# Kernel optimization log

Measured on AMD Instinct MI355X. Metric: run time of the kernel, lower is better.

## Reference

```python
import jax, jax.numpy as jnp
import numpy as np

LAM = 0.5


def _conv3x3(z, W):
    # z: [n, 2, h, w], W: [1, 2, 3, 3] (OIHW), padding=1, no bias
    return jax.lax.conv_general_dilated(
        z, W, window_strides=(1, 1), padding='SAME',
        dimension_numbers=('NCHW', 'OIHW', 'NCHW'))


def setup_inputs() -> dict:
    key = jax.random.key(0)
    k0, k1, k2, k3 = jax.random.split(key, 4)
    n, t, c, h, w = 32, 8, 128, 32, 32
    x = jax.random.normal(k0, (n, t, c, h, w), dtype=jnp.float32)
    alpha = jnp.full((1,), 0.5, dtype=jnp.float32)
    beta = jnp.full((1,), 0.5, dtype=jnp.float32)
    W_fc = jax.random.normal(k1, (t, t), dtype=jnp.float32) * (1.0 / np.sqrt(t))
    W_conv1 = jax.random.normal(k2, (1, 2, 3, 3), dtype=jnp.float32) * 0.2
    W_conv2 = jax.random.normal(k3, (1, 2, 3, 3), dtype=jnp.float32) * 0.2
    return {"x": x, "alpha": alpha, "beta": beta, "W_fc": W_fc,
            "W_conv1": W_conv1, "W_conv2": W_conv2}


def reference(x, alpha, beta, W_fc, W_conv1, W_conv2):
    n, t, c, h, w = x.shape
    # --- pooled time-channel map ---
    avg = jnp.mean(x, axis=(3, 4))            # [n,t,c]
    mx = jnp.max(x, axis=(3, 4))              # [n,t,c]
    map_add = 0.5 * (avg + mx) + alpha[0] * avg + beta[0] * mx
    # fc along time axis (Linear(t,t,bias=False) applied to [n,c,t]):
    # y[n,s,c] = sum_t map_add[n,t,c] * W_fc[s,t]
    map_add = jnp.einsum('ntc,st->nsc', map_add, W_fc)  # [n,t,c]

    kc = int(c * LAM)
    kt = int(t * LAM)
    # important channels: topk over channel axis, per timestep.
    # Faithful to the original: the fancy-index assignment unions the topk
    # selections over the batch, so the mask is batch-independent.
    _, idx_c = jax.lax.top_k(map_add, kc)                     # [n,t,kc]
    mask_c = jax.nn.one_hot(idx_c, c, dtype=x.dtype).max(axis=2).max(axis=0)  # [t,c]
    # important times: topk over time axis, per channel.
    _, idx_t = jax.lax.top_k(jnp.swapaxes(map_add, 1, 2), kt)  # [n,c,kt]
    mask_t = jax.nn.one_hot(idx_t, t, dtype=x.dtype).max(axis=2).max(axis=0).T  # [t,c]

    # torch.where((mask_c+mask_t)/2 == 0.5, 1, 0)  ==  XOR of the two masks
    im_tc = ((mask_c + mask_t) == 1.0).astype(x.dtype)  # [t,c]
    sub_tc = 1.0 - im_tc

    imf = x * im_tc[None, :, :, None, None]
    subf = x * sub_tc[None, :, :, None, None]
    imf = imf.reshape(n, t * c, h, w)
    subf = subf.reshape(n, t * c, h, w)

    im_avg = jnp.mean(imf, axis=1, keepdims=True) / LAM
    im_max = jnp.max(imf, axis=1, keepdims=True)
    sub_avg = jnp.mean(subf, axis=1, keepdims=True) / (1.0 - LAM)
    sub_max = jnp.max(subf, axis=1, keepdims=True)

    im_map = jax.nn.sigmoid(_conv3x3(jnp.concatenate([im_avg, im_max], axis=1), W_conv1))
    sub_map = jax.nn.sigmoid(_conv3x3(jnp.concatenate([sub_avg, sub_max], axis=1), W_conv2))

    out = im_map * imf + sub_map * subf                 # [n, t*c, h, w]
    return out.reshape(n, t, c, h, w)
```

## Files before the change

### kernel.cpp

```cpp
#include <hip/hip_runtime.h>
#include <math.h>

#define TC  1024
#define P_  1024
#define KC  64
#define KT  4

typedef float vfloat4 __attribute__((ext_vector_type(4)));


__global__ __launch_bounds__(256) void k1_reduce(const float* __restrict__ x,
                                                 float* __restrict__ avg,
                                                 float* __restrict__ mx,
                                                 int* __restrict__ masks) {
    int r = blockIdx.x;
    if (r == 0) {
        #pragma unroll
        for (int j = 0; j < 8; ++j) masks[j * 256 + threadIdx.x] = 0;
    }
    const float4* xp = (const float4*)(x + (size_t)r * P_);
    float4 v = xp[threadIdx.x];
    float s = (v.x + v.y) + (v.z + v.w);
    float m = fmaxf(fmaxf(v.x, v.y), fmaxf(v.z, v.w));
    #pragma unroll
    for (int off = 32; off > 0; off >>= 1) {
        s += __shfl_down(s, off);
        m  = fmaxf(m, __shfl_down(m, off));
    }
    __shared__ float ss[4], sm[4];
    int wid = threadIdx.x >> 6, lane = threadIdx.x & 63;
    if (lane == 0) { ss[wid] = s; sm[wid] = m; }
    __syncthreads();
    if (threadIdx.x == 0) {
        float ts = (ss[0] + ss[1]) + (ss[2] + ss[3]);
        float tm = fmaxf(fmaxf(sm[0], sm[1]), fmaxf(sm[2], sm[3]));
        avg[r] = ts * (1.0f / 1024.0f);
        mx[r]  = tm;
    }
}

__global__ __launch_bounds__(256) void k2_map(const float* __restrict__ avg,
                                              const float* __restrict__ mx,
                                              const float* __restrict__ alpha,
                                              const float* __restrict__ beta,
                                              const float* __restrict__ wfc,
                                              int* __restrict__ mask_c,
                                              int* __restrict__ mask_t) {
    __shared__ float m[TC], mf[TC], w[64];
    int n = blockIdx.x >> 3, tt = blockIdx.x & 7;
    float a0 = alpha[0], b0 = beta[0];
    if (threadIdx.x < 64) w[threadIdx.x] = wfc[threadIdx.x];
    for (int i = threadIdx.x; i < TC; i += 256) {
        float a = avg[n * TC + i], b = mx[n * TC + i];
        m[i] = 0.5f * (a + b) + a0 * a + b0 * b;
    }
    __syncthreads();
    for (int i = threadIdx.x; i < TC; i += 256) {
        int s = i >> 7, cc = i & 127;
        float acc = 0.0f;
        #pragma unroll
        for (int t2 = 0; t2 < 8; ++t2) acc += m[t2 * 128 + cc] * w[s * 8 + t2];
        mf[i] = acc;
    }
    __syncthreads();
    if (threadIdx.x < 128) {
        int cc = threadIdx.x, i = tt * 128 + cc;
        float v = mf[i];
        int rc = 0;
        #pragma unroll 16
        for (int c2 = 0; c2 < 128; ++c2) {
            float u = mf[tt * 128 + c2];
            rc += (u > v) || (u == v && c2 < cc);
        }
        if (rc < KC) mask_c[i] = 1;
        int rt = 0;
        #pragma unroll
        for (int t2 = 0; t2 < 8; ++t2) {
            float u = mf[t2 * 128 + cc];
            rt += (u > v) || (u == v && t2 < tt);
        }
        if (rt < KT) mask_t[i] = 1;
    }
}

__global__ __launch_bounds__(256) void k4_partial(const float* __restrict__ x,
                                                  const int* __restrict__ mask_c,
                                                  const int* __restrict__ mask_t,
                                                  float* __restrict__ flag_out,
                                                  float* __restrict__ part) {
    int b = blockIdx.x;
    int cq = b & 3, pq = (b >> 2) & 3, n = b >> 4;
    __shared__ float sf[256];
    __shared__ float4 red[4][4][64];
    {
        int i = threadIdx.x;
        int ch = cq * 256 + i;
        float f = ((mask_c[ch] != 0) != (mask_t[ch] != 0)) ? 1.0f : 0.0f;
        sf[i] = f;
        if (n == 0 && pq == 0) flag_out[ch] = f;
    }
    __syncthreads();
    int l = threadIdx.x & 63, cg = threadIdx.x >> 6;
    int f4p = pq * 64 + l;
    int ch0 = cq * 256 + cg * 64;
    const float4* xb = (const float4*)x + ((size_t)(n * TC + ch0)) * 256 + f4p;
    float4 ims  = {0.f, 0.f, 0.f, 0.f};
    float4 subs = {0.f, 0.f, 0.f, 0.f};
    float4 imm  = {-INFINITY, -INFINITY, -INFINITY, -INFINITY};
    float4 subm = {-INFINITY, -INFINITY, -INFINITY, -INFINITY};
    #pragma unroll 8
    for (int k = 0; k < 64; ++k) {
        float4 v = xb[(size_t)k * 256];
        float f = sf[cg * 64 + k];
        float iv;
        iv = v.x * f; ims.x += iv; imm.x = fmaxf(imm.x, iv);
        v.x -= iv;    subs.x += v.x; subm.x = fmaxf(subm.x, v.x);
        iv = v.y * f; ims.y += iv; imm.y = fmaxf(imm.y, iv);
        v.y -= iv;    subs.y += v.y; subm.y = fmaxf(subm.y, v.y);
        iv = v.z * f; ims.z += iv; imm.z = fmaxf(imm.z, iv);
        v.z -= iv;    subs.z += v.z; subm.z = fmaxf(subm.z, v.z);
        iv = v.w * f; ims.w += iv; imm.w = fmaxf(imm.w, iv);
        v.w -= iv;    subs.w += v.w; subm.w = fmaxf(subm.w, v.w);
    }
    red[0][cg][l] = ims;
    red[1][cg][l] = imm;
    red[2][cg][l] = subs;
    red[3][cg][l] = subm;
    __syncthreads();
    if (threadIdx.x < 64) {
        float4 s0 = red[0][0][l], s1 = red[1][0][l], s2 = red[2][0][l], s3 = red[3][0][l];
        #pragma unroll
        for (int g = 1; g < 4; ++g) {
            float4 a = red[0][g][l], bq = red[1][g][l], c = red[2][g][l], d = red[3][g][l];
            s0.x += a.x; s0.y += a.y; s0.z += a.z; s0.w += a.w;
            s1.x = fmaxf(s1.x, bq.x); s1.y = fmaxf(s1.y, bq.y);
            s1.z = fmaxf(s1.z, bq.z); s1.w = fmaxf(s1.w, bq.w);
            s2.x += c.x; s2.y += c.y; s2.z += c.z; s2.w += c.w;
            s3.x = fmaxf(s3.x, d.x); s3.y = fmaxf(s3.y, d.y);
            s3.z = fmaxf(s3.z, d.z); s3.w = fmaxf(s3.w, d.w);
        }
        float4* pp = (float4*)part + ((size_t)(cq * 32 + n) * 4) * 256 + f4p;
        pp[0]   = s0;
        pp[256] = s1;
        pp[512] = s2;
        pp[768] = s3;
    }
}

__global__ __launch_bounds__(1024) void k5_conv(const float* __restrict__ part,
                                                const float* __restrict__ w1,
                                                const float* __restrict__ w2,
                                                float* __restrict__ im_map,
                                                float* __restrict__ sub_map) {
    __shared__ float sp[4][P_];
    int n = blockIdx.x, p = threadIdx.x;
    float s_im = 0.f, s_sub = 0.f, m_im = -INFINITY, m_sub = -INFINITY;
    #pragma unroll
    for (int q = 0; q < 4; ++q) {
        size_t base = ((size_t)(q * 32 + n) * 4) * P_ + p;
        s_im  += part[base];
        m_im   = fmaxf(m_im, part[base + 1024]);
        s_sub += part[base + 2048];
        m_sub  = fmaxf(m_sub, part[base + 3072]);
    }
    sp[0][p] = s_im  * (2.0f / 1024.0f);
    sp[1][p] = m_im;
    sp[2][p] = s_sub * (2.0f / 1024.0f);
    sp[3][p] = m_sub;
    __syncthreads();
    int y = p >> 5, xx = p & 31;
    float acc1 = 0.0f, acc2 = 0.0f;
    #pragma unroll
    for (int i = 0; i < 2; ++i)
        #pragma unroll
        for (int dy = 0; dy < 3; ++dy) {
            int yy = y + dy - 1;
            if (yy < 0 || yy >= 32) continue;
            #pragma unroll
            for (int dx = 0; dx < 3; ++dx) {
                int xc = xx + dx - 1;
                if (xc < 0 || xc >= 32) continue;
                acc1 += sp[i][yy * 32 + xc]     * w1[i * 9 + dy * 3 + dx];
                acc2 += sp[2 + i][yy * 32 + xc] * w2[i * 9 + dy * 3 + dx];
            }
        }
    im_map[n * P_ + p]  = 1.0f / (1.0f + expf(-acc1));
    sub_map[n * P_ + p] = 1.0f / (1.0f + expf(-acc2));
}

__global__ __launch_bounds__(256) void k6_out(const float* __restrict__ x,
                                              const float* __restrict__ flag,
                                              const float* __restrict__ im_map,
                                              const float* __restrict__ sub_map,
                                              float* __restrict__ out) {
    int g   = blockIdx.x * 256 + threadIdx.x;
    int n   = g >> 16;
    int rem = g & 65535;
    int ch    = rem >> 8;
    int pixf4 = rem & 255;
    size_t base = ((size_t)n << 18) + rem;
    const float4* xp = (const float4*)x + base;
    const float4* imb  = (const float4*)im_map  + n * 256 + pixf4;
    const float4* subb = (const float4*)sub_map + n * 256 + pixf4;
    float4 im_v  = *imb;
    float4 sub_v = *subb;
    #pragma unroll
    for (int j = 0; j < 4; ++j) {
        float4 xv = xp[j * 65536];
        bool im = flag[ch + j * 256] != 0.0f;
        float4 mv = im ? im_v : sub_v;
        vfloat4 o;
        o.x = xv.x * mv.x; o.y = xv.y * mv.y; o.z = xv.z * mv.z; o.w = xv.w * mv.w;
        __builtin_nontemporal_store(o, (vfloat4*)out + base + (size_t)j * 65536);
    }
}

extern "C" void kernel_launch(void* const* d_in, const int* in_sizes, int n_in,
                              void* d_out, int out_size, void* d_ws, size_t ws_size,
                              hipStream_t stream) {
    const float* x     = (const float*)d_in[0];
    const float* alpha = (const float*)d_in[1];
    const float* beta  = (const float*)d_in[2];
    const float* wfc   = (const float*)d_in[3];
    const float* w1    = (const float*)d_in[4];
    const float* w2    = (const float*)d_in[5];
    float* out = (float*)d_out;
    float* ws  = (float*)d_ws;

    float* avg     = ws;
    float* mx      = ws + 32768;
    int*   mask_c  = (int*)(ws + 65536);
    int*   mask_t  = (int*)(ws + 66560);
    float* flag    = ws + 67584;
    float* im_map  = ws + 68608;
    float* sub_map = ws + 101376;
    float* part    = ws + 134144;

    k1_reduce <<<32768, 256, 0, stream>>>(x, avg, mx, mask_c);
    k2_map    <<<256,   256, 0, stream>>>(avg, mx, alpha, beta, wfc, mask_c, mask_t);
    k4_partial<<<512,   256, 0, stream>>>(x, mask_c, mask_t, flag, part);
    k5_conv   <<<32,   1024, 0, stream>>>(part, w1, w2, im_map, sub_map);
    k6_out    <<<8192,  256, 0, stream>>>(x, flag, im_map, sub_map, out);
}
```

Measured before the change: 96.59 us.

## Fuse conv kernel into partial-reduce via last-block atomic counter; one row per wave

```diff
diff --git a/kernel.cpp b/kernel.cpp
--- a/kernel.cpp
+++ b/kernel.cpp
@@ -12,30 +12,28 @@
 __global__ __launch_bounds__(256) void k1_reduce(const float* __restrict__ x,
                                                  float* __restrict__ avg,
                                                  float* __restrict__ mx,
-                                                 int* __restrict__ masks) {
-    int r = blockIdx.x;
-    if (r == 0) {
-        #pragma unroll
-        for (int j = 0; j < 8; ++j) masks[j * 256 + threadIdx.x] = 0;
-    }
-    const float4* xp = (const float4*)(x + (size_t)r * P_);
-    float4 v = xp[threadIdx.x];
-    float s = (v.x + v.y) + (v.z + v.w);
-    float m = fmaxf(fmaxf(v.x, v.y), fmaxf(v.z, v.w));
+                                                 int* __restrict__ zero_region) {
+    if (blockIdx.x == 0) {
+        for (int j = threadIdx.x; j < 2080; j += 256) zero_region[j] = 0;
+    }
+    int wid = threadIdx.x >> 6, lane = threadIdx.x & 63;
+    int r = blockIdx.x * 4 + wid;
+    const float4* xp = (const float4*)(x + (size_t)r * P_) + lane;
+    float4 a = xp[0], b = xp[64], c = xp[128], d = xp[192];
+    float s = ((a.x + a.y) + (a.z + a.w)) + ((b.x + b.y) + (b.z + b.w))
+            + ((c.x + c.y) + (c.z + c.w)) + ((d.x + d.y) + (d.z + d.w));
+    float m = fmaxf(fmaxf(fmaxf(fmaxf(a.x, a.y), fmaxf(a.z, a.w)),
+                          fmaxf(fmaxf(b.x, b.y), fmaxf(b.z, b.w))),
+                    fmaxf(fmaxf(fmaxf(c.x, c.y), fmaxf(c.z, c.w)),
+                          fmaxf(fmaxf(d.x, d.y), fmaxf(d.z, d.w))));
     #pragma unroll
     for (int off = 32; off > 0; off >>= 1) {
         s += __shfl_down(s, off);
         m  = fmaxf(m, __shfl_down(m, off));
     }
-    __shared__ float ss[4], sm[4];
-    int wid = threadIdx.x >> 6, lane = threadIdx.x & 63;
-    if (lane == 0) { ss[wid] = s; sm[wid] = m; }
-    __syncthreads();
-    if (threadIdx.x == 0) {
-        float ts = (ss[0] + ss[1]) + (ss[2] + ss[3]);
-        float tm = fmaxf(fmaxf(sm[0], sm[1]), fmaxf(sm[2], sm[3]));
-        avg[r] = ts * (1.0f / 1024.0f);
-        mx[r]  = tm;
+    if (lane == 0) {
+        avg[r] = s * (1.0f / 1024.0f);
+        mx[r]  = m;
     }
 }
 
@@ -86,12 +84,19 @@
 __global__ __launch_bounds__(256) void k4_partial(const float* __restrict__ x,
                                                   const int* __restrict__ mask_c,
                                                   const int* __restrict__ mask_t,
+                                                  int* __restrict__ cnt,
                                                   float* __restrict__ flag_out,
-                                                  float* __restrict__ part) {
+                                                  float* __restrict__ part,
+                                                  const float* __restrict__ w1,
+                                                  const float* __restrict__ w2,
+                                                  float* __restrict__ im_map,
+                                                  float* __restrict__ sub_map) {
     int b = blockIdx.x;
     int cq = b & 3, pq = (b >> 2) & 3, n = b >> 4;
     __shared__ float sf[256];
     __shared__ float4 red[4][4][64];
+    __shared__ float sp[4][P_];
+    __shared__ int is_last;
     {
         int i = threadIdx.x;
         int ch = cq * 256 + i;
@@ -145,47 +150,51 @@
         pp[512] = s2;
         pp[768] = s3;
     }
-}
-
-__global__ __launch_bounds__(1024) void k5_conv(const float* __restrict__ part,
-                                                const float* __restrict__ w1,
-                                                const float* __restrict__ w2,
-                                                float* __restrict__ im_map,
-                                                float* __restrict__ sub_map) {
-    __shared__ float sp[4][P_];
-    int n = blockIdx.x, p = threadIdx.x;
-    float s_im = 0.f, s_sub = 0.f, m_im = -INFINITY, m_sub = -INFINITY;
-    #pragma unroll
-    for (int q = 0; q < 4; ++q) {
-        size_t base = ((size_t)(q * 32 + n) * 4) * P_ + p;
-        s_im  += part[base];
-        m_im   = fmaxf(m_im, part[base + 1024]);
-        s_sub += part[base + 2048];
-        m_sub  = fmaxf(m_sub, part[base + 3072]);
-    }
-    sp[0][p] = s_im  * (2.0f / 1024.0f);
-    sp[1][p] = m_im;
-    sp[2][p] = s_sub * (2.0f / 1024.0f);
-    sp[3][p] = m_sub;
-    __syncthreads();
-    int y = p >> 5, xx = p & 31;
-    float acc1 = 0.0f, acc2 = 0.0f;
-    #pragma unroll
-    for (int i = 0; i < 2; ++i)
-        #pragma unroll
-        for (int dy = 0; dy < 3; ++dy) {
-            int yy = y + dy - 1;
-            if (yy < 0 || yy >= 32) continue;
+    __threadfence();
+    __syncthreads();
+    if (threadIdx.x == 0) {
+        int old = atomicAdd(&cnt[n], 1);
+        is_last = (old == 15);
+    }
+    __syncthreads();
+    if (!is_last) return;
+    __threadfence();
+    for (int p = threadIdx.x; p < P_; p += 256) {
+        float s_im = 0.f, s_sub = 0.f, m_im = -INFINITY, m_sub = -INFINITY;
+        #pragma unroll
+        for (int q = 0; q < 4; ++q) {
+            size_t base = ((size_t)(q * 32 + n) * 4) * P_ + p;
+            s_im  += part[base];
+            m_im   = fmaxf(m_im, part[base + 1024]);
+            s_sub += part[base + 2048];
+            m_sub  = fmaxf(m_sub, part[base + 3072]);
+        }
+        sp[0][p] = s_im  * (2.0f / 1024.0f);
+        sp[1][p] = m_im;
+        sp[2][p] = s_sub * (2.0f / 1024.0f);
+        sp[3][p] = m_sub;
+    }
+    __syncthreads();
+    for (int p = threadIdx.x; p < P_; p += 256) {
+        int y = p >> 5, xx = p & 31;
+        float acc1 = 0.0f, acc2 = 0.0f;
+        #pragma unroll
+        for (int i = 0; i < 2; ++i)
             #pragma unroll
-            for (int dx = 0; dx < 3; ++dx) {
-                int xc = xx + dx - 1;
-                if (xc < 0 || xc >= 32) continue;
-                acc1 += sp[i][yy * 32 + xc]     * w1[i * 9 + dy * 3 + dx];
-                acc2 += sp[2 + i][yy * 32 + xc] * w2[i * 9 + dy * 3 + dx];
+            for (int dy = 0; dy < 3; ++dy) {
+                int yy = y + dy - 1;
+                if (yy < 0 || yy >= 32) continue;
+                #pragma unroll
+                for (int dx = 0; dx < 3; ++dx) {
+                    int xc = xx + dx - 1;
+                    if (xc < 0 || xc >= 32) continue;
+                    acc1 += sp[i][yy * 32 + xc]     * w1[i * 9 + dy * 3 + dx];
+                    acc2 += sp[2 + i][yy * 32 + xc] * w2[i * 9 + dy * 3 + dx];
+                }
             }
-        }
-    im_map[n * P_ + p]  = 1.0f / (1.0f + expf(-acc1));
-    sub_map[n * P_ + p] = 1.0f / (1.0f + expf(-acc2));
+        im_map[n * P_ + p]  = 1.0f / (1.0f + expf(-acc1));
+        sub_map[n * P_ + p] = 1.0f / (1.0f + expf(-acc2));
+    }
 }
 
 __global__ __launch_bounds__(256) void k6_out(const float* __restrict__ x,
@@ -231,14 +240,15 @@
     float* mx      = ws + 32768;
     int*   mask_c  = (int*)(ws + 65536);
     int*   mask_t  = (int*)(ws + 66560);
-    float* flag    = ws + 67584;
-    float* im_map  = ws + 68608;
-    float* sub_map = ws + 101376;
-    float* part    = ws + 134144;
-
-    k1_reduce <<<32768, 256, 0, stream>>>(x, avg, mx, mask_c);
+    int*   cnt     = (int*)(ws + 67584);
+    float* flag    = ws + 67616;
+    float* im_map  = ws + 68640;
+    float* sub_map = ws + 101408;
+    float* part    = ws + 134176;
+
+    k1_reduce <<<8192,  256, 0, stream>>>(x, avg, mx, mask_c);
     k2_map    <<<256,   256, 0, stream>>>(avg, mx, alpha, beta, wfc, mask_c, mask_t);
-    k4_partial<<<512,   256, 0, stream>>>(x, mask_c, mask_t, flag, part);
-    k5_conv   <<<32,   1024, 0, stream>>>(part, w1, w2, im_map, sub_map);
+    k4_partial<<<512,   256, 0, stream>>>(x, mask_c, mask_t, cnt, flag, part,
+                                          w1, w2, im_map, sub_map);
     k6_out    <<<8192,  256, 0, stream>>>(x, flag, im_map, sub_map, out);
 }
```

Measured after the change: 150.1 us. +55.4%, slower.
